# Performance work log

Measured on AMD Instinct MI355X. Metric: run time of the kernel, lower is better.

Reference implementation:

```python
import jax, jax.numpy as jnp
import numpy as np

GRID_MIN, GRID_MAX, GRID_SIZE = -4.0, 4.0, 12
BANDWIDTH = (GRID_MAX - GRID_MIN) / max(GRID_SIZE - 1, 1)  # 8/11


def setup_inputs() -> dict:
    key = jax.random.key(0)
    k1, k2, k3, k4 = jax.random.split(key, 4)
    B, I, O, G = 16384, 512, 512, GRID_SIZE
    x = jax.random.normal(k1, (B, I), dtype=jnp.float32)
    coeff = jax.random.normal(k2, (I, O, G), dtype=jnp.float32) * 0.05
    base_w = jax.random.normal(k3, (O, I), dtype=jnp.float32) * (1.0 / np.sqrt(I))
    base_b = jax.random.normal(k4, (O,), dtype=jnp.float32) * 0.01
    centers = jnp.linspace(GRID_MIN, GRID_MAX, G, dtype=jnp.float32)
    return {"x": x, "coeff": coeff, "base_w": base_w, "base_b": base_b, "centers": centers}


def reference(x, coeff, base_w, base_b, centers):
    # RBF basis: [B, I, G]
    diff = (x[..., None] - centers) / jnp.float32(BANDWIDTH)
    basis = jnp.exp(-0.5 * diff * diff)
    # spline contraction over in_dim and grid: [B, O]
    spline = jnp.einsum('big,iog->bo', basis, coeff)
    # residual base linear (torch Linear: x @ W^T + b)
    return spline + x @ base_w.T + base_b
```

## Files before the change

### kernel.cpp

```cpp
#include <hip/hip_runtime.h>
#include <hip/hip_bf16.h>


#define M_DIM 16384
#define N_DIM 512
#define I_DIM 512
#define KTOT  6656
#define NSTEP 104

typedef short short8 __attribute__((ext_vector_type(8)));
typedef float f32x16 __attribute__((ext_vector_type(16)));
typedef unsigned int u32x4 __attribute__((ext_vector_type(4)));

#define CVTPK(dst, lo, hi) \
  asm("v_cvt_pk_bf16_f32 %0, %1, %2" : "=v"(dst) : "v"(lo), "v"(hi))

__device__ __forceinline__ unsigned short f2bf(float f) {
  union { float f; unsigned int u; } c; c.f = f;
  unsigned int r = (c.u + 0x7FFFu + ((c.u >> 16) & 1)) >> 16;
  return (unsigned short)r;
}

__global__ __launch_bounds__(256) void prep_w(const float* __restrict__ coeff,
                                              const float* __restrict__ base_w,
                                              unsigned short* __restrict__ Wb2) {
  int t = blockIdx.x * 256 + threadIdx.x;
  int e0 = (t & 1) * 4;
  int go = t >> 1;
  int o  = go & 511;
  int g  = go >> 9;
  int k4 = g * 8 + e0;
  int ic = k4 / 832;
  int rem = k4 - ic * 832;
  int slot = rem >> 6;
  int ii = rem & 63;
  int i = ic * 64 + ii;
  float v0, v1, v2, v3;
  if (slot == 0) {
    const float4 bw = *(const float4*)(base_w + (size_t)o * I_DIM + i);
    v0 = bw.x; v1 = bw.y; v2 = bw.z; v3 = bw.w;
  } else {
    int gg = slot - 1;
    const float* cp = coeff + (size_t)i * (N_DIM * 12) + o * 12 + gg;
    v0 = cp[0]; v1 = cp[6144]; v2 = cp[2 * 6144]; v3 = cp[3 * 6144];
  }
  ushort4 s;
  s.x = f2bf(v0); s.y = f2bf(v1); s.z = f2bf(v2); s.w = f2bf(v3);
  *(ushort4*)(Wb2 + (size_t)go * 8 + e0) = s;
}

__global__ __launch_bounds__(512, 2) void kan_gemm(const float* __restrict__ x,
                                                   const unsigned short* __restrict__ Wb2,
                                                   const float* __restrict__ bias,
                                                   float* __restrict__ out) {
  __shared__ unsigned short Asw[2][8 * 128 * 8];
  __shared__ unsigned short Bsw[3][8 * 256 * 8];

  const int tid  = threadIdx.x;
  const int lane = tid & 63;
  const int wid  = tid >> 6;
  const int wm   = wid >> 2, wn = wid & 3;

  const int rb = blockIdx.x >> 1;
  const int cb = blockIdx.x & 1;
  const int M0 = rb * 128;
  const int N0 = cb * 256;

  const int arow = tid & 127;
  const int kgp  = tid >> 7;
  const float* xg = x + (size_t)(M0 + arow) * I_DIM + kgp * 16;
  const int aoff0 = ((kgp * 2) * 128 + arow) * 16;
  const int aoff1 = ((kgp * 2 + 1) * 128 + arow) * 16;

  const unsigned short* bsrc[4];
  int bdst[4];
#pragma unroll
  for (int q = 0; q < 4; ++q) {
    bsrc[q] = Wb2 + ((size_t)wid * 512 + N0 + q * 64 + lane) * 8;
    bdst[q] = (wid * 256 + q * 64) * 16;
  }

  const int l31 = lane & 31;
  const int aBase = ((lane >> 5) * 128 + wm * 64 + l31) * 16;
  const int bBase = ((lane >> 5) * 256 + wn * 64 + l31) * 16;

  f32x16 acc[2][2];
#pragma unroll
  for (int i = 0; i < 2; ++i)
#pragma unroll
    for (int j = 0; j < 2; ++j)
#pragma unroll
      for (int r = 0; r < 16; ++r) acc[i][j][r] = 0.f;

  float4 xq[4];
#pragma unroll
  for (int q = 0; q < 4; ++q) xq[q] = *(const float4*)(xg + q * 4);
  float bb[16], ff[16];
  int gic = 0;

  float f0[16];
#pragma unroll
  for (int q = 0; q < 4; ++q) {
    f0[q*4+0] = xq[q].x; f0[q*4+1] = xq[q].y; f0[q*4+2] = xq[q].z; f0[q*4+3] = xq[q].w;
  }
#pragma unroll
  for (int q = 0; q < 4; ++q) xq[q] = *(const float4*)(xg + 64 + q * 4);
  gic = 1;
#pragma unroll
  for (int q = 0; q < 4; ++q)
    __builtin_amdgcn_global_load_lds(
        (const __attribute__((address_space(1))) void*)(bsrc[q]),
        (__attribute__((address_space(3))) void*)((char*)&Bsw[0][0] + bdst[q]), 16, 0, 0);
#pragma unroll
  for (int q = 0; q < 4; ++q)
    __builtin_amdgcn_global_load_lds(
        (const __attribute__((address_space(1))) void*)(bsrc[q] + 32768),
        (__attribute__((address_space(3))) void*)((char*)&Bsw[1][0] + bdst[q]), 16, 0, 0);
  {
    unsigned int w[8];
#pragma unroll
    for (int j = 0; j < 8; ++j) CVTPK(w[j], f0[2*j], f0[2*j+1]);
    char* pA = (char*)&Asw[0][0];
    *(u32x4*)(pA + aoff0) = (u32x4){w[0], w[1], w[2], w[3]};
    *(u32x4*)(pA + aoff1) = (u32x4){w[4], w[5], w[6], w[7]};
#pragma unroll
    for (int j = 0; j < 16; ++j) {
      float u = fmaf(f0[j], 1.375f, 5.5f);
      bb[j] = exp2f(-0.72134752044448170f * u * u);
      ff[j] = exp2f(fmaf(u, 1.44269504088896340f, -0.72134752044448170f));
    }
  }
  __builtin_amdgcn_sched_barrier(0);
  asm volatile("s_waitcnt vmcnt(4) lgkmcnt(0)" ::: "memory");
  __builtin_amdgcn_sched_barrier(0);
  __builtin_amdgcn_s_barrier();
  __builtin_amdgcn_sched_barrier(0);

  int nslot = 1;
  int cur3  = 0;
  for (int t = 0; t < NSTEP; ++t) {
    const bool emit = (t < NSTEP - 1);
    const bool s0   = (nslot == 0);
    bool reload = false;
    float f[16];

    if (emit && s0) {
#pragma unroll
      for (int q = 0; q < 4; ++q) {
        f[q*4+0] = xq[q].x; f[q*4+1] = xq[q].y; f[q*4+2] = xq[q].z; f[q*4+3] = xq[q].w;
      }
      if (gic < 7) {
        const float* xn = xg + (size_t)(gic + 1) * 64;
#pragma unroll
        for (int q = 0; q < 4; ++q) xq[q] = *(const float4*)(xn + q * 4);
        reload = true;
      }
      ++gic;
    }

    if (t < NSTEP - 2) {
      const int nx3 = (cur3 >= 1) ? cur3 - 1 : 2;
      char* bb2 = (char*)&Bsw[nx3][0];
      const size_t ko = (size_t)(t + 2) * 32768;
#pragma unroll
      for (int q = 0; q < 4; ++q)
        __builtin_amdgcn_global_load_lds(
            (const __attribute__((address_space(1))) void*)(bsrc[q] + ko),
            (__attribute__((address_space(3))) void*)(bb2 + bdst[q]), 16, 0, 0);
    }

    if (emit) {
      char* pA = (char*)&Asw[(t + 1) & 1][0];
      unsigned int w[8];
      if (s0) {
#pragma unroll
        for (int j = 0; j < 8; ++j) CVTPK(w[j], f[2*j], f[2*j+1]);
        *(u32x4*)(pA + aoff0) = (u32x4){w[0], w[1], w[2], w[3]};
        *(u32x4*)(pA + aoff1) = (u32x4){w[4], w[5], w[6], w[7]};
#pragma unroll
        for (int j = 0; j < 16; ++j) {
          float u = fmaf(f[j], 1.375f, 5.5f);
          bb[j] = exp2f(-0.72134752044448170f * u * u);
          ff[j] = exp2f(fmaf(u, 1.44269504088896340f, -0.72134752044448170f));
        }
      } else {
#pragma unroll
        for (int j = 0; j < 8; ++j) CVTPK(w[j], bb[2*j], bb[2*j+1]);
        *(u32x4*)(pA + aoff0) = (u32x4){w[0], w[1], w[2], w[3]};
        *(u32x4*)(pA + aoff1) = (u32x4){w[4], w[5], w[6], w[7]};
#pragma unroll
        for (int j = 0; j < 16; ++j) {
          bb[j] *= ff[j];
          ff[j] *= 0.36787944117144233f;
        }
      }
    }

    {
      const char* pA = (const char*)&Asw[t & 1][0];
      const char* pB = (const char*)&Bsw[cur3][0];
      __builtin_amdgcn_s_setprio(1);
#pragma unroll
      for (int s = 0; s < 4; ++s) {
        const char* a = pA + aBase + s * 4096;
        const char* b = pB + bBase + s * 8192;
        short8 a0 = *(const short8*)(a);
        short8 a1 = *(const short8*)(a + 512);
        short8 b0 = *(const short8*)(b);
        short8 b1 = *(const short8*)(b + 512);
        acc[0][0] = __builtin_amdgcn_mfma_f32_32x32x16_bf16(a0, b0, acc[0][0], 0, 0, 0);
        acc[0][1] = __builtin_amdgcn_mfma_f32_32x32x16_bf16(a0, b1, acc[0][1], 0, 0, 0);
        acc[1][0] = __builtin_amdgcn_mfma_f32_32x32x16_bf16(a1, b0, acc[1][0], 0, 0, 0);
        acc[1][1] = __builtin_amdgcn_mfma_f32_32x32x16_bf16(a1, b1, acc[1][1], 0, 0, 0);
      }
      __builtin_amdgcn_s_setprio(0);
    }

    __builtin_amdgcn_sched_barrier(0);
    if (reload) {
      asm volatile("s_waitcnt vmcnt(8) lgkmcnt(0)" ::: "memory");
    } else {
      asm volatile("s_waitcnt vmcnt(4) lgkmcnt(0)" ::: "memory");
    }
    __builtin_amdgcn_sched_barrier(0);
    __builtin_amdgcn_s_barrier();
    __builtin_amdgcn_sched_barrier(0);

    nslot = (nslot == 12) ? 0 : nslot + 1;
    cur3  = (cur3 == 2) ? 0 : cur3 + 1;
  }

  float bv[2];
#pragma unroll
  for (int fn = 0; fn < 2; ++fn) bv[fn] = bias[N0 + wn * 64 + fn * 32 + l31];
  const int rbase = (lane >> 5) * 4;
#pragma unroll
  for (int fm = 0; fm < 2; ++fm) {
#pragma unroll
    for (int fn = 0; fn < 2; ++fn) {
      const size_t cix = (size_t)(N0 + wn * 64 + fn * 32 + l31);
#pragma unroll
      for (int r = 0; r < 16; ++r) {
        int row = M0 + wm * 64 + fm * 32 + (r & 3) + 8 * (r >> 2) + rbase;
        out[(size_t)row * N_DIM + cix] = acc[fm][fn][r] + bv[fn];
      }
    }
  }
}

extern "C" void kernel_launch(void* const* d_in, const int* in_sizes, int n_in,
                              void* d_out, int out_size, void* d_ws, size_t ws_size,
                              hipStream_t stream) {
  const float* x      = (const float*)d_in[0];
  const float* coeff  = (const float*)d_in[1];
  const float* base_w = (const float*)d_in[2];
  const float* base_b = (const float*)d_in[3];
  unsigned short* Wb2 = (unsigned short*)d_ws;

  prep_w<<<3328, 256, 0, stream>>>(coeff, base_w, Wb2);
  kan_gemm<<<256, 512, 0, stream>>>(x, Wb2, base_b, (float*)d_out);
}
```

Measured before the change: 149.8 us.

## Hoist LDS fragment loads and move basis math after MFMAs

The main loop now reads all A/B LDS fragments for the step up front, then issues the next B stage and the A-tile emit, and only then runs the MFMA chain. The exp/basis recurrence update is moved after the MFMAs so it can overlap with matrix work, and the x prefetch for the next chunk is moved to a different slot in the 13-step cycle. Scheduling barriers are removed and the loop is forced not to unroll, leaving instruction placement to the compiler. This uses more registers to hold the fragments, and the reordered waitcnt logic has to stay correct.

```diff
diff --git a/kernel.cpp b/kernel.cpp
--- a/kernel.cpp
+++ b/kernel.cpp
@@ -2,7 +2,6 @@
 #include <hip/hip_bf16.h>
 
 
-#define M_DIM 16384
 #define N_DIM 512
 #define I_DIM 512
 #define KTOT  6656
@@ -60,6 +59,7 @@
   const int lane = tid & 63;
   const int wid  = tid >> 6;
   const int wm   = wid >> 2, wn = wid & 3;
+  const int l31  = lane & 31, hl = lane >> 5;
 
   const int rb = blockIdx.x >> 1;
   const int cb = blockIdx.x & 1;
@@ -80,9 +80,18 @@
     bdst[q] = (wid * 256 + q * 64) * 16;
   }
 
-  const int l31 = lane & 31;
-  const int aBase = ((lane >> 5) * 128 + wm * 64 + l31) * 16;
-  const int bBase = ((lane >> 5) * 256 + wn * 64 + l31) * 16;
+#define STAGE(T_, RING_) do {                                                  \
+    const size_t ko_ = (size_t)(T_) * 32768;                                   \
+    char* d_ = (char*)&Bsw[RING_][0];                                          \
+    _Pragma("unroll")                                                          \
+    for (int q_ = 0; q_ < 4; ++q_)                                             \
+      __builtin_amdgcn_global_load_lds(                                        \
+          (const __attribute__((address_space(1))) void*)(bsrc[q_] + ko_),     \
+          (__attribute__((address_space(3))) void*)(d_ + bdst[q_]), 16, 0, 0); \
+  } while (0)
+
+  const int aBase = (hl * 128 + wm * 64 + l31) * 16;
+  const int bBase = (hl * 256 + wn * 64 + l31) * 16;
 
   f32x16 acc[2][2];
 #pragma unroll
@@ -92,102 +101,96 @@
 #pragma unroll
       for (int r = 0; r < 16; ++r) acc[i][j][r] = 0.f;
 
-  float4 xq[4];
-#pragma unroll
-  for (int q = 0; q < 4; ++q) xq[q] = *(const float4*)(xg + q * 4);
   float bb[16], ff[16];
-  int gic = 0;
-
-  float f0[16];
-#pragma unroll
-  for (int q = 0; q < 4; ++q) {
-    f0[q*4+0] = xq[q].x; f0[q*4+1] = xq[q].y; f0[q*4+2] = xq[q].z; f0[q*4+3] = xq[q].w;
-  }
-#pragma unroll
-  for (int q = 0; q < 4; ++q) xq[q] = *(const float4*)(xg + 64 + q * 4);
-  gic = 1;
-#pragma unroll
-  for (int q = 0; q < 4; ++q)
-    __builtin_amdgcn_global_load_lds(
-        (const __attribute__((address_space(1))) void*)(bsrc[q]),
-        (__attribute__((address_space(3))) void*)((char*)&Bsw[0][0] + bdst[q]), 16, 0, 0);
-#pragma unroll
-  for (int q = 0; q < 4; ++q)
-    __builtin_amdgcn_global_load_lds(
-        (const __attribute__((address_space(1))) void*)(bsrc[q] + 32768),
-        (__attribute__((address_space(3))) void*)((char*)&Bsw[1][0] + bdst[q]), 16, 0, 0);
+  float4 xh[4];
+
+#pragma unroll
+  for (int q = 0; q < 4; ++q) xh[q] = *(const float4*)(xg + q * 4);
+  STAGE(0, 0);
+  STAGE(1, 1);
   {
+    float f[16];
+#pragma unroll
+    for (int q = 0; q < 4; ++q) {
+      f[q*4+0] = xh[q].x; f[q*4+1] = xh[q].y; f[q*4+2] = xh[q].z; f[q*4+3] = xh[q].w;
+    }
     unsigned int w[8];
 #pragma unroll
-    for (int j = 0; j < 8; ++j) CVTPK(w[j], f0[2*j], f0[2*j+1]);
-    char* pA = (char*)&Asw[0][0];
-    *(u32x4*)(pA + aoff0) = (u32x4){w[0], w[1], w[2], w[3]};
-    *(u32x4*)(pA + aoff1) = (u32x4){w[4], w[5], w[6], w[7]};
+    for (int j = 0; j < 8; ++j) CVTPK(w[j], f[2*j], f[2*j+1]);
+    char* pAe = (char*)&Asw[0][0];
+    *(u32x4*)(pAe + aoff0) = (u32x4){w[0], w[1], w[2], w[3]};
+    *(u32x4*)(pAe + aoff1) = (u32x4){w[4], w[5], w[6], w[7]};
 #pragma unroll
     for (int j = 0; j < 16; ++j) {
-      float u = fmaf(f0[j], 1.375f, 5.5f);
+      float u = fmaf(f[j], 1.375f, 5.5f);
       bb[j] = exp2f(-0.72134752044448170f * u * u);
       ff[j] = exp2f(fmaf(u, 1.44269504088896340f, -0.72134752044448170f));
     }
   }
-  __builtin_amdgcn_sched_barrier(0);
   asm volatile("s_waitcnt vmcnt(4) lgkmcnt(0)" ::: "memory");
-  __builtin_amdgcn_sched_barrier(0);
   __builtin_amdgcn_s_barrier();
-  __builtin_amdgcn_sched_barrier(0);
-
-  int nslot = 1;
-  int cur3  = 0;
+
+  int cur3 = 0, tm13 = 0, cchunk = 1;
+#pragma unroll 1
   for (int t = 0; t < NSTEP; ++t) {
-    const bool emit = (t < NSTEP - 1);
-    const bool s0   = (nslot == 0);
-    bool reload = false;
-    float f[16];
-
-    if (emit && s0) {
-#pragma unroll
-      for (int q = 0; q < 4; ++q) {
-        f[q*4+0] = xq[q].x; f[q*4+1] = xq[q].y; f[q*4+2] = xq[q].z; f[q*4+3] = xq[q].w;
+    const char* pA  = (const char*)&Asw[t & 1][0];
+    const char* pB  = (const char*)&Bsw[cur3][0];
+    char*       pAe = (char*)&Asw[(t + 1) & 1][0];
+
+    short8 av[2][4], bv[2][4];
+#pragma unroll
+    for (int s = 0; s < 4; ++s) {
+      av[0][s] = *(const short8*)(pA + aBase + s * 4096);
+      av[1][s] = *(const short8*)(pA + aBase + s * 4096 + 512);
+      bv[0][s] = *(const short8*)(pB + bBase + s * 8192);
+      bv[1][s] = *(const short8*)(pB + bBase + s * 8192 + 512);
+    }
+
+    const bool doStage = (t < NSTEP - 2);
+    {
+      int nring = cur3 + 2; if (nring >= 3) nring -= 3;
+      if (doStage) STAGE(t + 2, nring);
+    }
+
+    if (t < NSTEP - 1) {
+      unsigned int w[8];
+      if (tm13 == 12) {
+        float f[16];
+#pragma unroll
+        for (int q = 0; q < 4; ++q) {
+          f[q*4+0] = xh[q].x; f[q*4+1] = xh[q].y; f[q*4+2] = xh[q].z; f[q*4+3] = xh[q].w;
+        }
+#pragma unroll
+        for (int j = 0; j < 8; ++j) CVTPK(w[j], f[2*j], f[2*j+1]);
+      } else {
+#pragma unroll
+        for (int j = 0; j < 8; ++j) CVTPK(w[j], bb[2*j], bb[2*j+1]);
       }
-      if (gic < 7) {
-        const float* xn = xg + (size_t)(gic + 1) * 64;
-#pragma unroll
-        for (int q = 0; q < 4; ++q) xq[q] = *(const float4*)(xn + q * 4);
-        reload = true;
-      }
-      ++gic;
-    }
+      *(u32x4*)(pAe + aoff0) = (u32x4){w[0], w[1], w[2], w[3]};
+      *(u32x4*)(pAe + aoff1) = (u32x4){w[4], w[5], w[6], w[7]};
+    }
+
+    __builtin_amdgcn_s_setprio(1);
+#pragma unroll
+    for (int s = 0; s < 4; ++s) {
+      acc[0][0] = __builtin_amdgcn_mfma_f32_32x32x16_bf16(av[0][s], bv[0][s], acc[0][0], 0, 0, 0);
+      acc[0][1] = __builtin_amdgcn_mfma_f32_32x32x16_bf16(av[0][s], bv[1][s], acc[0][1], 0, 0, 0);
+      acc[1][0] = __builtin_amdgcn_mfma_f32_32x32x16_bf16(av[1][s], bv[0][s], acc[1][0], 0, 0, 0);
+      acc[1][1] = __builtin_amdgcn_mfma_f32_32x32x16_bf16(av[1][s], bv[1][s], acc[1][1], 0, 0, 0);
+    }
+    __builtin_amdgcn_s_setprio(0);
 
     if (t < NSTEP - 2) {
-      const int nx3 = (cur3 >= 1) ? cur3 - 1 : 2;
-      char* bb2 = (char*)&Bsw[nx3][0];
-      const size_t ko = (size_t)(t + 2) * 32768;
-#pragma unroll
-      for (int q = 0; q < 4; ++q)
-        __builtin_amdgcn_global_load_lds(
-            (const __attribute__((address_space(1))) void*)(bsrc[q] + ko),
-            (__attribute__((address_space(3))) void*)(bb2 + bdst[q]), 16, 0, 0);
-    }
-
-    if (emit) {
-      char* pA = (char*)&Asw[(t + 1) & 1][0];
-      unsigned int w[8];
-      if (s0) {
-#pragma unroll
-        for (int j = 0; j < 8; ++j) CVTPK(w[j], f[2*j], f[2*j+1]);
-        *(u32x4*)(pA + aoff0) = (u32x4){w[0], w[1], w[2], w[3]};
-        *(u32x4*)(pA + aoff1) = (u32x4){w[4], w[5], w[6], w[7]};
+      if (tm13 == 12) {
 #pragma unroll
         for (int j = 0; j < 16; ++j) {
-          float u = fmaf(f[j], 1.375f, 5.5f);
+          float xv = (j < 4 ? (&xh[0].x)[j] : j < 8 ? (&xh[1].x)[j-4]
+                     : j < 12 ? (&xh[2].x)[j-8] : (&xh[3].x)[j-12]);
+          float u = fmaf(xv, 1.375f, 5.5f);
           bb[j] = exp2f(-0.72134752044448170f * u * u);
           ff[j] = exp2f(fmaf(u, 1.44269504088896340f, -0.72134752044448170f));
         }
-      } else {
-#pragma unroll
-        for (int j = 0; j < 8; ++j) CVTPK(w[j], bb[2*j], bb[2*j+1]);
-        *(u32x4*)(pA + aoff0) = (u32x4){w[0], w[1], w[2], w[3]};
-        *(u32x4*)(pA + aoff1) = (u32x4){w[4], w[5], w[6], w[7]};
+      } else if (tm13 != 11) {
 #pragma unroll
         for (int j = 0; j < 16; ++j) {
           bb[j] *= ff[j];
@@ -195,54 +198,40 @@
         }
       }
     }
-
-    {
-      const char* pA = (const char*)&Asw[t & 1][0];
-      const char* pB = (const char*)&Bsw[cur3][0];
-      __builtin_amdgcn_s_setprio(1);
-#pragma unroll
-      for (int s = 0; s < 4; ++s) {
-        const char* a = pA + aBase + s * 4096;
-        const char* b = pB + bBase + s * 8192;
-        short8 a0 = *(const short8*)(a);
-        short8 a1 = *(const short8*)(a + 512);
-        short8 b0 = *(const short8*)(b);
-        short8 b1 = *(const short8*)(b + 512);
-        acc[0][0] = __builtin_amdgcn_mfma_f32_32x32x16_bf16(a0, b0, acc[0][0], 0, 0, 0);
-        acc[0][1] = __builtin_amdgcn_mfma_f32_32x32x16_bf16(a0, b1, acc[0][1], 0, 0, 0);
-        acc[1][0] = __builtin_amdgcn_mfma_f32_32x32x16_bf16(a1, b0, acc[1][0], 0, 0, 0);
-        acc[1][1] = __builtin_amdgcn_mfma_f32_32x32x16_bf16(a1, b1, acc[1][1], 0, 0, 0);
-      }
-      __builtin_amdgcn_s_setprio(0);
-    }
-
-    __builtin_amdgcn_sched_barrier(0);
-    if (reload) {
+    bool xstep = (tm13 == 2) && (cchunk < 8);
+    if (xstep) {
+      const float* xn = xg + (size_t)cchunk * 64;
+#pragma unroll
+      for (int q = 0; q < 4; ++q) xh[q] = *(const float4*)(xn + q * 4);
+      ++cchunk;
+    }
+
+    if (!doStage) {
+      asm volatile("s_waitcnt vmcnt(0) lgkmcnt(0)" ::: "memory");
+    } else if (xstep) {
       asm volatile("s_waitcnt vmcnt(8) lgkmcnt(0)" ::: "memory");
     } else {
       asm volatile("s_waitcnt vmcnt(4) lgkmcnt(0)" ::: "memory");
     }
-    __builtin_amdgcn_sched_barrier(0);
     __builtin_amdgcn_s_barrier();
-    __builtin_amdgcn_sched_barrier(0);
-
-    nslot = (nslot == 12) ? 0 : nslot + 1;
-    cur3  = (cur3 == 2) ? 0 : cur3 + 1;
-  }
-
-  float bv[2];
-#pragma unroll
-  for (int fn = 0; fn < 2; ++fn) bv[fn] = bias[N0 + wn * 64 + fn * 32 + l31];
-  const int rbase = (lane >> 5) * 4;
-#pragma unroll
-  for (int fm = 0; fm < 2; ++fm) {
-#pragma unroll
-    for (int fn = 0; fn < 2; ++fn) {
-      const size_t cix = (size_t)(N0 + wn * 64 + fn * 32 + l31);
+
+    if (++tm13 == 13) tm13 = 0;
+    cur3 = (cur3 == 2) ? 0 : cur3 + 1;
+  }
+
+  float bvv[2];
+#pragma unroll
+  for (int fo = 0; fo < 2; ++fo) bvv[fo] = bias[N0 + wn * 64 + fo * 32 + l31];
+  const int rbase = 4 * hl;
+#pragma unroll
+  for (int fb = 0; fb < 2; ++fb) {
+#pragma unroll
+    for (int fo = 0; fo < 2; ++fo) {
+      const size_t cix = (size_t)(N0 + wn * 64 + fo * 32 + l31);
 #pragma unroll
       for (int r = 0; r < 16; ++r) {
-        int row = M0 + wm * 64 + fm * 32 + (r & 3) + 8 * (r >> 2) + rbase;
-        out[(size_t)row * N_DIM + cix] = acc[fm][fn][r] + bv[fn];
+        int row = M0 + wm * 64 + fb * 32 + (r & 3) + 8 * (r >> 2) + rbase;
+        out[(size_t)row * N_DIM + cix] = acc[fb][fo][r] + bvv[fo];
       }
     }
   }
```

Measured after the change: 157.2 us. 5.0% more time.
